# Kernel tuning notes

Measured on AMD Instinct MI355X. Metric: run time of the kernel, lower is better.

## Reference

```python
import jax, jax.numpy as jnp
import numpy as np

IN_FEATURES = 1024
OUT_FEATURES = 1024
B, S = 8, 4096


def setup_inputs() -> dict:
    key = jax.random.key(0)
    kx, kw = jax.random.split(key)
    x = jax.random.normal(kx, (B, S, IN_FEATURES), dtype=jnp.float32)
    # weight initialized as randn * 0.1, shape [out_features, in_features]
    weight = jax.random.normal(kw, (OUT_FEATURES, IN_FEATURES), dtype=jnp.float32) * 0.1
    bias = jnp.zeros((OUT_FEATURES,), dtype=jnp.float32)
    return {"x": x, "weight": weight, "bias": bias}


def reference(x, weight, bias):
    # BitNetLinear eval-mode forward.
    # Weight quantization to ternary {-1, 0, +1} with mean-abs scale.
    w_scale = jnp.mean(jnp.abs(weight))  # scalar
    q_weight = jnp.sign(weight) * (jnp.abs(weight) > 0.5 * w_scale).astype(weight.dtype)
    # Activation quantization to int8 range with global abs-max scale.
    i_scale = jnp.max(jnp.abs(x)) / 127.0  # scalar
    q_input = jnp.clip(jnp.round(x / i_scale), -128.0, 127.0)
    # Float GEMM on quantized values, then dequant with both scales.
    out = jnp.einsum('bsk,ok->bso', q_input, q_weight) * w_scale * i_scale
    out = out + bias  # bias added after dequant, matching the torch code
    return out
```

## Files before the change

### kernel.cpp

```cpp
#include <hip/hip_runtime.h>
#include <stdint.h>


#define MK_M 32768
#define MK_K 1024
#define MK_N 1024

typedef __attribute__((ext_vector_type(4))) int int32x4;

#define WS_MAXP_OFF 64
#define WS_PART_OFF 8448
#define WS_QW_OFF 16384
#define WS_NEEDED (WS_QW_OFF + (1 << 20))

__global__ void kprep(const float4* __restrict__ x4, const float4* __restrict__ w4,
                      float* __restrict__ maxp, double* __restrict__ partials, long n4x) {
    const int bid = blockIdx.x;
    if (bid < 2048) {
        float m = 0.f;
        const long stride = 2048L * 256;
        for (long i = (long)bid * 256 + threadIdx.x; i < n4x; i += stride) {
            float4 v = x4[i];
            m = fmaxf(m, fmaxf(fmaxf(fabsf(v.x), fabsf(v.y)), fmaxf(fabsf(v.z), fabsf(v.w))));
        }
        #pragma unroll
        for (int off = 1; off < 64; off <<= 1) m = fmaxf(m, __shfl_xor(m, off));
        __shared__ float sm[4];
        int lane = threadIdx.x & 63, wid = threadIdx.x >> 6;
        if (lane == 0) sm[wid] = m;
        __syncthreads();
        if (threadIdx.x == 0) maxp[bid] = fmaxf(fmaxf(sm[0], sm[1]), fmaxf(sm[2], sm[3]));
    } else {
        double s = 0.0;
        for (int i = (bid - 2048) * 256 + threadIdx.x; i < (1 << 18); i += 64 * 256) {
            float4 v = w4[i];
            s += (double)fabsf(v.x);
            s += (double)fabsf(v.y);
            s += (double)fabsf(v.z);
            s += (double)fabsf(v.w);
        }
        __shared__ double sd[256];
        sd[threadIdx.x] = s;
        __syncthreads();
        for (int h = 128; h > 0; h >>= 1) {
            if ((int)threadIdx.x < h) sd[threadIdx.x] += sd[threadIdx.x + h];
            __syncthreads();
        }
        if (threadIdx.x == 0) partials[bid - 2048] = sd[0];
    }
}

__global__ void kquant_w(const float4* __restrict__ w4, unsigned* __restrict__ qw,
                         const double* __restrict__ partials, float* __restrict__ wscp) {
    __shared__ double sws;
    if (threadIdx.x < 64) {
        double s = partials[threadIdx.x];
        #pragma unroll
        for (int off = 1; off < 64; off <<= 1) s += __shfl_xor(s, off);
        if (threadIdx.x == 0) sws = s;
    }
    __syncthreads();
    float wsc = (float)(sws / 1048576.0);
    if (blockIdx.x == 0 && threadIdx.x == 0) *wscp = wsc;
    float thr = 0.5f * wsc;
    int stride = gridDim.x * blockDim.x;
    for (int i = blockIdx.x * blockDim.x + threadIdx.x; i < (1 << 18); i += stride) {
        float4 v = w4[i];
        int q0 = (fabsf(v.x) > thr) ? (v.x > 0.f ? 1 : -1) : 0;
        int q1 = (fabsf(v.y) > thr) ? (v.y > 0.f ? 1 : -1) : 0;
        int q2 = (fabsf(v.z) > thr) ? (v.z > 0.f ? 1 : -1) : 0;
        int q3 = (fabsf(v.w) > thr) ? (v.w > 0.f ? 1 : -1) : 0;
        qw[i] = (q0 & 0xff) | ((q1 & 0xff) << 8) | ((q2 & 0xff) << 16) | ((q3 & 0xff) << 24);
    }
}

__global__ __launch_bounds__(512, 2) void kfused(
    const float* __restrict__ x, const char* __restrict__ qw,
    const float* __restrict__ bias, const float* __restrict__ wscp,
    const float* __restrict__ maxp, float* __restrict__ out)
{
    __shared__ __align__(16) char As[2][8192];
    __shared__ __align__(16) char Bs[3][16384];
    __shared__ float smx[8];

    const int t = threadIdx.x;
    const int l = t & 63;
    const int w = t >> 6;
    const int wm = w >> 2;
    const int wn = w & 3;

    const int bid = blockIdx.x;
    const int wg = (bid & 7) * 128 + (bid >> 3);
    const int tm = wg >> 2, tn = wg & 3;
    const long m0 = (long)tm * 128;
    const int n0 = tn * 256;

    float m = 0.f;
    #pragma unroll
    for (int j = 0; j < 4; ++j) m = fmaxf(m, maxp[t + 512 * j]);
    #pragma unroll
    for (int off = 1; off < 64; off <<= 1) m = fmaxf(m, __shfl_xor(m, off));
    if (l == 0) smx[w] = m;
    __syncthreads();
    const float mm = fmaxf(fmaxf(fmaxf(smx[0], smx[1]), fmaxf(smx[2], smx[3])),
                           fmaxf(fmaxf(smx[4], smx[5]), fmaxf(smx[6], smx[7])));
    const float isc = mm / 127.0f;
    const float rin = 1.0f / isc;

    const int arow = t >> 2;
    const int ac = t & 3;
    const float4* gA4 = (const float4*)(x + (m0 + arow) * MK_K + ac * 16);
    const int adsw = (ac ^ ((arow >> 1) & 3));
    char* const adst0 = (char*)As[0] + arow * 64 + adsw * 16;
    char* const adst1 = (char*)As[1] + arow * 64 + adsw * 16;

    const int gch = (t & 3) ^ ((t >> 3) & 3);
    const char* gBt = qw + ((long)n0 + (t >> 2)) * MK_K + gch * 16;
    auto stageB = [&](int kt1, int b) {
        char* dst = (char*)Bs[b] + t * 16;
        const char* src = gBt + kt1 * 64;
        __builtin_amdgcn_global_load_lds(
            (const __attribute__((address_space(1))) void*)src,
            (__attribute__((address_space(3))) void*)dst, 16, 0, 0);
        __builtin_amdgcn_global_load_lds(
            (const __attribute__((address_space(1))) void*)(src + 128L * MK_K),
            (__attribute__((address_space(3))) void*)(dst + 8192), 16, 0, 0);
    };

    float4 ar0, ar1, ar2, ar3;
    auto issueA = [&](int kt1) {
        ar0 = gA4[kt1 * 16 + 0];
        ar1 = gA4[kt1 * 16 + 1];
        ar2 = gA4[kt1 * 16 + 2];
        ar3 = gA4[kt1 * 16 + 3];
    };
    auto quantA = [&](char* dst) {
        int p[4];
        float4 vv[4] = {ar0, ar1, ar2, ar3};
        #pragma unroll
        for (int q = 0; q < 4; ++q) {
            int i0 = (int)rintf(vv[q].x * rin);
            int i1 = (int)rintf(vv[q].y * rin);
            int i2 = (int)rintf(vv[q].z * rin);
            int i3 = (int)rintf(vv[q].w * rin);
            p[q] = (i0 & 0xff) | ((i1 & 0xff) << 8) | ((i2 & 0xff) << 16) | ((i3 & 0xff) << 24);
        }
        int32x4 pk = {p[0], p[1], p[2], p[3]};
        *(int32x4*)dst = pk;
    };

    int32x4 acc[4][4];
    #pragma unroll
    for (int mi = 0; mi < 4; ++mi)
        #pragma unroll
        for (int ni = 0; ni < 4; ++ni) acc[mi][ni] = (int32x4)0;

    issueA(0);
    stageB(0, 0);
    asm volatile("s_waitcnt vmcnt(2)" ::: "memory");
    quantA(adst0);
    issueA(1);
    stageB(1, 1);

    for (int kt = 0; kt < 16; ++kt) {
        if (kt < 15) asm volatile("s_waitcnt vmcnt(2) lgkmcnt(0)" ::: "memory");
        else         asm volatile("s_waitcnt vmcnt(0) lgkmcnt(0)" ::: "memory");
        __builtin_amdgcn_s_barrier();

        if (kt < 15) quantA((kt & 1) ? adst0 : adst1);
        if (kt < 14) {
            issueA(kt + 2);
            stageB(kt + 2, (kt + 2) % 3);
        }

        const char* bufA = As[kt & 1];
        const char* bufB = Bs[kt % 3];
        int32x4 af[4], bf[4];
        #pragma unroll
        for (int i = 0; i < 4; ++i) {
            int row = wm * 64 + i * 16 + (l & 15);
            int ch = (l >> 4) ^ ((row >> 1) & 3);
            af[i] = *(const int32x4*)(bufA + row * 64 + ch * 16);
        }
        #pragma unroll
        for (int i = 0; i < 4; ++i) {
            int row = wn * 64 + i * 16 + (l & 15);
            int ch = (l >> 4) ^ ((row >> 1) & 3);
            bf[i] = *(const int32x4*)(bufB + row * 64 + ch * 16);
        }
        __builtin_amdgcn_s_setprio(1);
        #pragma unroll
        for (int mi = 0; mi < 4; ++mi)
            #pragma unroll
            for (int ni = 0; ni < 4; ++ni)
                acc[mi][ni] = __builtin_amdgcn_mfma_i32_16x16x64_i8(
                    af[mi], bf[ni], acc[mi][ni], 0, 0, 0);
        __builtin_amdgcn_s_setprio(0);
    }

    const float wsc = *wscp;
    const int crow = (l >> 4) * 4;
    const int ccol = l & 15;
    #pragma unroll
    for (int mi = 0; mi < 4; ++mi) {
        #pragma unroll
        for (int ni = 0; ni < 4; ++ni) {
            long r0 = m0 + wm * 64 + mi * 16 + crow;
            int c = n0 + wn * 64 + ni * 16 + ccol;
            float b = bias[c];
            #pragma unroll
            for (int j = 0; j < 4; ++j) {
                out[(r0 + j) * MK_N + c] = ((float)acc[mi][ni][j] * wsc) * isc + b;
            }
        }
    }
}

extern "C" void kernel_launch(void* const* d_in, const int* in_sizes, int n_in,
                              void* d_out, int out_size, void* d_ws, size_t ws_size,
                              hipStream_t stream) {
    const float* x = (const float*)d_in[0];
    const float* wt = (const float*)d_in[1];
    const float* bias = (const float*)d_in[2];
    float* out = (float*)d_out;

    if (ws_size < WS_NEEDED) return;

    char* ws = (char*)d_ws;
    float* wscp = (float*)(ws + 0);
    float* maxp = (float*)(ws + WS_MAXP_OFF);
    double* partials = (double*)(ws + WS_PART_OFF);
    char* qw = ws + WS_QW_OFF;

    const long n_x = (long)in_sizes[0];
    const long n4_x = n_x >> 2;

    kprep<<<2112, 256, 0, stream>>>((const float4*)x, (const float4*)wt, maxp, partials, n4_x);
    kquant_w<<<256, 256, 0, stream>>>((const float4*)wt, (unsigned*)qw, partials, wscp);

    const int grid = (MK_M / 128) * (MK_N / 256);
    kfused<<<grid, 512, 0, stream>>>(x, qw, bias, wscp, maxp, out);
}
```

Before: 103.2 us.

## Shrink fused GEMM tile to 64x256 with 256 threads and double-buffered B

The fused quantize-GEMM kernel moves from 128x256 tiles with 512 threads to 64x256 tiles with 256 threads. Each wave now covers all 64 rows and a 64-column slice. The B pipeline drops from three stages with two-ahead prefetch to two stages with one-ahead staging and a full vmcnt(0) wait every iteration. The max-scale reduction now runs per wave without a block barrier. Each block reuses more of B per A byte and more blocks fit per CU, but B traffic per output doubles and the shallower pipeline exposes more global-load latency.

```diff
diff --git a/kernel.cpp b/kernel.cpp
--- a/kernel.cpp
+++ b/kernel.cpp
@@ -74,43 +74,36 @@
     }
 }
 
-__global__ __launch_bounds__(512, 2) void kfused(
+__global__ __launch_bounds__(256, 4) void kfused(
     const float* __restrict__ x, const char* __restrict__ qw,
     const float* __restrict__ bias, const float* __restrict__ wscp,
     const float* __restrict__ maxp, float* __restrict__ out)
 {
-    __shared__ __align__(16) char As[2][8192];
-    __shared__ __align__(16) char Bs[3][16384];
-    __shared__ float smx[8];
+    __shared__ __align__(16) char As[2][4096];
+    __shared__ __align__(16) char Bs[2][16384];
 
     const int t = threadIdx.x;
     const int l = t & 63;
     const int w = t >> 6;
-    const int wm = w >> 2;
-    const int wn = w & 3;
 
     const int bid = blockIdx.x;
-    const int wg = (bid & 7) * 128 + (bid >> 3);
+    const int wg = (bid & 7) * 256 + (bid >> 3);
     const int tm = wg >> 2, tn = wg & 3;
-    const long m0 = (long)tm * 128;
+    const long m0 = (long)tm * 64;
     const int n0 = tn * 256;
 
     float m = 0.f;
     #pragma unroll
-    for (int j = 0; j < 4; ++j) m = fmaxf(m, maxp[t + 512 * j]);
+    for (int j = 0; j < 32; ++j) m = fmaxf(m, maxp[l + 64 * j]);
     #pragma unroll
     for (int off = 1; off < 64; off <<= 1) m = fmaxf(m, __shfl_xor(m, off));
-    if (l == 0) smx[w] = m;
-    __syncthreads();
-    const float mm = fmaxf(fmaxf(fmaxf(smx[0], smx[1]), fmaxf(smx[2], smx[3])),
-                           fmaxf(fmaxf(smx[4], smx[5]), fmaxf(smx[6], smx[7])));
-    const float isc = mm / 127.0f;
+    const float isc = m / 127.0f;
     const float rin = 1.0f / isc;
 
     const int arow = t >> 2;
     const int ac = t & 3;
     const float4* gA4 = (const float4*)(x + (m0 + arow) * MK_K + ac * 16);
-    const int adsw = (ac ^ ((arow >> 1) & 3));
+    const int adsw = ac ^ ((arow >> 1) & 3);
     char* const adst0 = (char*)As[0] + arow * 64 + adsw * 16;
     char* const adst1 = (char*)As[1] + arow * 64 + adsw * 16;
 
@@ -119,12 +112,12 @@
     auto stageB = [&](int kt1, int b) {
         char* dst = (char*)Bs[b] + t * 16;
         const char* src = gBt + kt1 * 64;
-        __builtin_amdgcn_global_load_lds(
-            (const __attribute__((address_space(1))) void*)src,
-            (__attribute__((address_space(3))) void*)dst, 16, 0, 0);
-        __builtin_amdgcn_global_load_lds(
-            (const __attribute__((address_space(1))) void*)(src + 128L * MK_K),
-            (__attribute__((address_space(3))) void*)(dst + 8192), 16, 0, 0);
+        #pragma unroll
+        for (int u = 0; u < 4; ++u) {
+            __builtin_amdgcn_global_load_lds(
+                (const __attribute__((address_space(1))) void*)(src + (long)u * 64 * MK_K),
+                (__attribute__((address_space(3))) void*)(dst + u * 4096), 16, 0, 0);
+        }
     };
 
     float4 ar0, ar1, ar2, ar3;
@@ -156,35 +149,33 @@
         for (int ni = 0; ni < 4; ++ni) acc[mi][ni] = (int32x4)0;
 
     issueA(0);
-    stageB(0, 0);
-    asm volatile("s_waitcnt vmcnt(2)" ::: "memory");
+    asm volatile("s_waitcnt vmcnt(0)" ::: "memory");
     quantA(adst0);
     issueA(1);
-    stageB(1, 1);
+    stageB(0, 0);
 
     for (int kt = 0; kt < 16; ++kt) {
-        if (kt < 15) asm volatile("s_waitcnt vmcnt(2) lgkmcnt(0)" ::: "memory");
-        else         asm volatile("s_waitcnt vmcnt(0) lgkmcnt(0)" ::: "memory");
+        asm volatile("s_waitcnt vmcnt(0) lgkmcnt(0)" ::: "memory");
         __builtin_amdgcn_s_barrier();
 
-        if (kt < 15) quantA((kt & 1) ? adst0 : adst1);
-        if (kt < 14) {
-            issueA(kt + 2);
-            stageB(kt + 2, (kt + 2) % 3);
-        }
+        if (kt < 15) {
+            quantA((kt & 1) ? adst0 : adst1);
+            stageB(kt + 1, (kt + 1) & 1);
+        }
+        if (kt < 14) issueA(kt + 2);
 
         const char* bufA = As[kt & 1];
-        const char* bufB = Bs[kt % 3];
+        const char* bufB = Bs[kt & 1];
         int32x4 af[4], bf[4];
         #pragma unroll
         for (int i = 0; i < 4; ++i) {
-            int row = wm * 64 + i * 16 + (l & 15);
+            int row = i * 16 + (l & 15);
             int ch = (l >> 4) ^ ((row >> 1) & 3);
             af[i] = *(const int32x4*)(bufA + row * 64 + ch * 16);
         }
         #pragma unroll
         for (int i = 0; i < 4; ++i) {
-            int row = wn * 64 + i * 16 + (l & 15);
+            int row = w * 64 + i * 16 + (l & 15);
             int ch = (l >> 4) ^ ((row >> 1) & 3);
             bf[i] = *(const int32x4*)(bufB + row * 64 + ch * 16);
         }
@@ -205,8 +196,8 @@
     for (int mi = 0; mi < 4; ++mi) {
         #pragma unroll
         for (int ni = 0; ni < 4; ++ni) {
-            long r0 = m0 + wm * 64 + mi * 16 + crow;
-            int c = n0 + wn * 64 + ni * 16 + ccol;
+            long r0 = m0 + mi * 16 + crow;
+            int c = n0 + w * 64 + ni * 16 + ccol;
             float b = bias[c];
             #pragma unroll
             for (int j = 0; j < 4; ++j) {
@@ -238,6 +229,6 @@
     kprep<<<2112, 256, 0, stream>>>((const float4*)x, (const float4*)wt, maxp, partials, n4_x);
     kquant_w<<<256, 256, 0, stream>>>((const float4*)wt, (unsigned*)qw, partials, wscp);
 
-    const int grid = (MK_M / 128) * (MK_N / 256);
-    kfused<<<grid, 512, 0, stream>>>(x, qw, bias, wscp, maxp, out);
-}
+    const int grid = (MK_M / 64) * (MK_N / 256);
+    kfused<<<grid, 256, 0, stream>>>(x, qw, bias, wscp, maxp, out);
+}
```

Result: slower. 112.9 us (+9.4%).

## Shrink N tile to 128 and load ternary weights straight into registers

Applied to the files above, without the earlier changes.

The output tile shrinks from 128x256 to 128x128, which doubles the grid and halves the accumulators per wave. The weight operand is no longer staged through LDS with async global-to-LDS copies. Each wave now reads its B fragments directly from global memory into registers, double-buffered and one k-step ahead, and the k-loop is fully unrolled with a plain __syncthreads. This cuts LDS footprint and register pressure, but the float32 activation tile is now read and quantized twice as often across N-tiles, and B fragment loads hit global/L2 with no sharing between waves in the workgroup.

```diff
diff --git a/kernel.cpp b/kernel.cpp
--- a/kernel.cpp
+++ b/kernel.cpp
@@ -80,7 +80,6 @@
     const float* __restrict__ maxp, float* __restrict__ out)
 {
     __shared__ __align__(16) char As[2][8192];
-    __shared__ __align__(16) char Bs[3][16384];
     __shared__ float smx[8];
 
     const int t = threadIdx.x;
@@ -90,10 +89,10 @@
     const int wn = w & 3;
 
     const int bid = blockIdx.x;
-    const int wg = (bid & 7) * 128 + (bid >> 3);
-    const int tm = wg >> 2, tn = wg & 3;
+    const int wg = (bid & 7) * 256 + (bid >> 3);
+    const int tm = wg >> 3, tn = wg & 7;
     const long m0 = (long)tm * 128;
-    const int n0 = tn * 256;
+    const int n0 = tn * 128;
 
     float m = 0.f;
     #pragma unroll
@@ -113,19 +112,6 @@
     const int adsw = (ac ^ ((arow >> 1) & 3));
     char* const adst0 = (char*)As[0] + arow * 64 + adsw * 16;
     char* const adst1 = (char*)As[1] + arow * 64 + adsw * 16;
-
-    const int gch = (t & 3) ^ ((t >> 3) & 3);
-    const char* gBt = qw + ((long)n0 + (t >> 2)) * MK_K + gch * 16;
-    auto stageB = [&](int kt1, int b) {
-        char* dst = (char*)Bs[b] + t * 16;
-        const char* src = gBt + kt1 * 64;
-        __builtin_amdgcn_global_load_lds(
-            (const __attribute__((address_space(1))) void*)src,
-            (__attribute__((address_space(3))) void*)dst, 16, 0, 0);
-        __builtin_amdgcn_global_load_lds(
-            (const __attribute__((address_space(1))) void*)(src + 128L * MK_K),
-            (__attribute__((address_space(3))) void*)(dst + 8192), 16, 0, 0);
-    };
 
     float4 ar0, ar1, ar2, ar3;
     auto issueA = [&](int kt1) {
@@ -149,54 +135,65 @@
         *(int32x4*)dst = pk;
     };
 
-    int32x4 acc[4][4];
-    #pragma unroll
-    for (int mi = 0; mi < 4; ++mi)
-        #pragma unroll
-        for (int ni = 0; ni < 4; ++ni) acc[mi][ni] = (int32x4)0;
+    const char* bq = qw + (long)(n0 + wn * 32 + (l & 15)) * MK_K + (l >> 4) * 16;
+
+    int32x4 acc[4][2];
+    #pragma unroll
+    for (int mi = 0; mi < 4; ++mi) {
+        acc[mi][0] = (int32x4)0;
+        acc[mi][1] = (int32x4)0;
+    }
 
     issueA(0);
-    stageB(0, 0);
-    asm volatile("s_waitcnt vmcnt(2)" ::: "memory");
     quantA(adst0);
     issueA(1);
-    stageB(1, 1);
-
-    for (int kt = 0; kt < 16; ++kt) {
-        if (kt < 15) asm volatile("s_waitcnt vmcnt(2) lgkmcnt(0)" ::: "memory");
-        else         asm volatile("s_waitcnt vmcnt(0) lgkmcnt(0)" ::: "memory");
-        __builtin_amdgcn_s_barrier();
-
-        if (kt < 15) quantA((kt & 1) ? adst0 : adst1);
-        if (kt < 14) {
-            issueA(kt + 2);
-            stageB(kt + 2, (kt + 2) % 3);
-        }
-
-        const char* bufA = As[kt & 1];
-        const char* bufB = Bs[kt % 3];
-        int32x4 af[4], bf[4];
-        #pragma unroll
-        for (int i = 0; i < 4; ++i) {
-            int row = wm * 64 + i * 16 + (l & 15);
-            int ch = (l >> 4) ^ ((row >> 1) & 3);
-            af[i] = *(const int32x4*)(bufA + row * 64 + ch * 16);
-        }
-        #pragma unroll
-        for (int i = 0; i < 4; ++i) {
-            int row = wn * 64 + i * 16 + (l & 15);
-            int ch = (l >> 4) ^ ((row >> 1) & 3);
-            bf[i] = *(const int32x4*)(bufB + row * 64 + ch * 16);
-        }
-        __builtin_amdgcn_s_setprio(1);
-        #pragma unroll
-        for (int mi = 0; mi < 4; ++mi)
-            #pragma unroll
-            for (int ni = 0; ni < 4; ++ni)
-                acc[mi][ni] = __builtin_amdgcn_mfma_i32_16x16x64_i8(
-                    af[mi], bf[ni], acc[mi][ni], 0, 0, 0);
-        __builtin_amdgcn_s_setprio(0);
-    }
+    int32x4 bfP[2], bfQ[2];
+    bfP[0] = *(const int32x4*)(bq);
+    bfP[1] = *(const int32x4*)(bq + 16 * MK_K);
+
+#define R15_BODY(KT, BC, BN)                                                      \
+    {                                                                             \
+        __syncthreads();                                                          \
+        if ((KT) < 15) quantA(((KT) & 1) ? adst0 : adst1);                        \
+        if ((KT) < 14) issueA((KT) + 2);                                          \
+        const char* bufA = As[(KT) & 1];                                          \
+        int32x4 af[4];                                                            \
+        _Pragma("unroll")                                                         \
+        for (int i = 0; i < 4; ++i) {                                             \
+            int row = wm * 64 + i * 16 + (l & 15);                                \
+            int ch = (l >> 4) ^ ((row >> 1) & 3);                                 \
+            af[i] = *(const int32x4*)(bufA + row * 64 + ch * 16);                 \
+        }                                                                         \
+        if ((KT) < 15) {                                                          \
+            BN[0] = *(const int32x4*)(bq + ((KT) + 1) * 64);                      \
+            BN[1] = *(const int32x4*)(bq + 16 * MK_K + ((KT) + 1) * 64);          \
+        }                                                                         \
+        __builtin_amdgcn_s_setprio(1);                                            \
+        _Pragma("unroll")                                                         \
+        for (int mi = 0; mi < 4; ++mi) {                                          \
+            acc[mi][0] = __builtin_amdgcn_mfma_i32_16x16x64_i8(af[mi], BC[0], acc[mi][0], 0, 0, 0); \
+            acc[mi][1] = __builtin_amdgcn_mfma_i32_16x16x64_i8(af[mi], BC[1], acc[mi][1], 0, 0, 0); \
+        }                                                                         \
+        __builtin_amdgcn_s_setprio(0);                                            \
+    }
+
+    R15_BODY(0,  bfP, bfQ)
+    R15_BODY(1,  bfQ, bfP)
+    R15_BODY(2,  bfP, bfQ)
+    R15_BODY(3,  bfQ, bfP)
+    R15_BODY(4,  bfP, bfQ)
+    R15_BODY(5,  bfQ, bfP)
+    R15_BODY(6,  bfP, bfQ)
+    R15_BODY(7,  bfQ, bfP)
+    R15_BODY(8,  bfP, bfQ)
+    R15_BODY(9,  bfQ, bfP)
+    R15_BODY(10, bfP, bfQ)
+    R15_BODY(11, bfQ, bfP)
+    R15_BODY(12, bfP, bfQ)
+    R15_BODY(13, bfQ, bfP)
+    R15_BODY(14, bfP, bfQ)
+    R15_BODY(15, bfQ, bfP)
+#undef R15_BODY
 
     const float wsc = *wscp;
     const int crow = (l >> 4) * 4;
@@ -204,9 +201,9 @@
     #pragma unroll
     for (int mi = 0; mi < 4; ++mi) {
         #pragma unroll
-        for (int ni = 0; ni < 4; ++ni) {
+        for (int ni = 0; ni < 2; ++ni) {
             long r0 = m0 + wm * 64 + mi * 16 + crow;
-            int c = n0 + wn * 64 + ni * 16 + ccol;
+            int c = n0 + wn * 32 + ni * 16 + ccol;
             float b = bias[c];
             #pragma unroll
             for (int j = 0; j < 4; ++j) {
@@ -238,6 +235,6 @@
     kprep<<<2112, 256, 0, stream>>>((const float4*)x, (const float4*)wt, maxp, partials, n4_x);
     kquant_w<<<256, 256, 0, stream>>>((const float4*)wt, (unsigned*)qw, partials, wscp);
 
-    const int grid = (MK_M / 128) * (MK_N / 256);
+    const int grid = (MK_M / 128) * (MK_N / 128);
     kfused<<<grid, 512, 0, stream>>>(x, qw, bias, wscp, maxp, out);
 }
```

Result: slower. 161.2 us (+56.3%).
